# Kernel tuning notes

Hardware: AMD Instinct MI355X
Metric: run time of the kernel (lower is better)

## Reference

```python
import jax, jax.numpy as jnp
import numpy as np

IN = 128      # input_size
HID = 64      # fast_net hidden width
NFW = IN * HID + HID  # 8256 flat fast weights (layer1 then layer2)
B = 256


def setup_inputs() -> dict:
    key = jax.random.key(0)
    k1, k2, k3, k4 = jax.random.split(key, 4)
    x = jax.random.normal(k1, (B, 1, IN), dtype=jnp.float32)
    # updater network weights: Linear(IN, 2*NFW, bias=False) then Linear(2*NFW, NFW, bias=False)
    W1 = jax.random.normal(k2, (2 * NFW, IN), dtype=jnp.float32) * 0.02
    W2 = jax.random.normal(k3, (NFW, 2 * NFW), dtype=jnp.float32) * 0.02
    # initial flat fast weights, in (0,1) since the update squashes there
    fw0 = jax.random.uniform(k4, (NFW,), dtype=jnp.float32)
    return {"x": x, "W1": W1, "W2": W2, "fw0": fw0}


def reference(x, W1, W2, fw0):
    xs = x[:, 0, :]  # [B, IN]
    # updater network has no weight updates itself -> batch the two matmuls
    U = (xs @ W1.T) @ W2.T  # [B, NFW] per-sample weight updates
    gain, shift = jnp.float32(10.0), jnp.float32(0.5)

    def step(fw, inp):
        x_i, u_i = inp
        # update_func: 1 / (1 + exp(-10*(w + u - 0.5)))
        fw = jax.nn.sigmoid(gain * (fw + u_i - shift))
        w1 = fw[: IN * HID].reshape(HID, IN)   # fast layer 1 [HID, IN]
        w2 = fw[IN * HID:].reshape(1, HID)     # fast layer 2 [1, HID]
        pred = w2 @ jax.nn.relu(w1 @ x_i)      # [1]
        return fw, pred

    _, preds = jax.lax.scan(step, fw0, (xs, U))  # sequential over batch, state persists
    return preds  # [B, 1]
```

## Files before the change

kernel.cpp:

```cpp
#include <hip/hip_runtime.h>
#include <hip/hip_bf16.h>

#define IN_DIM 128
#define HID    64
#define NFW    8256
#define BATCH  256
#define K2     16512
#define BM     96
#define NMB    86
#define KSPLIT 6
#define NT_PER 43
#define GRID_M 516

typedef float f32x4 __attribute__((ext_vector_type(4)));
typedef short bf16x8 __attribute__((ext_vector_type(8)));

__device__ __forceinline__ unsigned int f2bf(float f) {
    union { float f; unsigned int u; } v; v.f = f;
    return (v.u + 0x7FFFu + ((v.u >> 16) & 1u)) >> 16;
}

__global__ __launch_bounds__(256) void k_prep_w1t(const float* __restrict__ W1,
                                                  unsigned short* __restrict__ W1T) {
    __shared__ float tile[64][IN_DIM + 1];
    const int kt = blockIdx.x;
    const int t  = threadIdx.x;
    const float* src = W1 + (size_t)kt * 64 * IN_DIM;
#pragma unroll
    for (int p = 0; p < 8; ++p) {
        int c4 = p * 256 + t;
        int e = c4 * 4;
        int row = e >> 7, col = e & 127;
        f32x4 v = *reinterpret_cast<const f32x4*>(src + row * IN_DIM + col);
        tile[row][col+0] = v.x; tile[row][col+1] = v.y;
        tile[row][col+2] = v.z; tile[row][col+3] = v.w;
    }
    __syncthreads();
    unsigned short* dst = W1T + (size_t)kt * (IN_DIM * 64);
#pragma unroll
    for (int it = 0; it < 4; ++it) {
        int c = it * 256 + t;
        int n = c >> 3, kl0 = (c & 7) * 8;
        uint4 w;
        w.x = f2bf(tile[kl0+0][n]) | (f2bf(tile[kl0+1][n]) << 16);
        w.y = f2bf(tile[kl0+2][n]) | (f2bf(tile[kl0+3][n]) << 16);
        w.z = f2bf(tile[kl0+4][n]) | (f2bf(tile[kl0+5][n]) << 16);
        w.w = f2bf(tile[kl0+6][n]) | (f2bf(tile[kl0+7][n]) << 16);
        *reinterpret_cast<uint4*>(dst + c * 8) = w;
    }
}

__global__ __launch_bounds__(256, 2) void k_gemm_M(const float* __restrict__ W2,
                                                   const unsigned short* __restrict__ W1T,
                                                   float* __restrict__ Mpart) {
    __shared__ __align__(16) unsigned char smem[57344];
    float* trs = reinterpret_cast<float*>(smem);

    const int t = threadIdx.x;
    const int lane = t & 63, wid = t >> 6;
    const int wm = wid >> 1, wn = wid & 1;
    const int l15 = lane & 15, l4 = (lane >> 4) & 3;

    const int b = blockIdx.x;
    const int xcd = b & 7, slot = b >> 3;
    const int p = (xcd < 4) ? (xcd * 65 + slot) : (260 + (xcd - 4) * 64 + slot);
    const int ks = p / NMB, mb = p % NMB;

    const int m0 = mb * BM;
    const int g0 = ks * NT_PER;
    const int kt0 = (p * 7) % NT_PER;

    const int ar  = t >> 3;
    const int ac  = (t & 7) * 8;
    const int asw = (ar & 7) << 4;
    const float* abase = W2 + (size_t)(m0 + ar) * K2 + (size_t)g0 * 64 + ac;
    const int bn  = t >> 1;
    const int bsw = (bn & 7) << 4;
    const unsigned short* bbase = W1T + (size_t)g0 * 8192 + bn * 64 + (t & 1) * 32;

    f32x4 sa0, sa1, sa2, sa3, sa4, sa5;
    uint4 sb0, sb1, sb2, sb3;
    f32x4 acc[3][4];
#pragma unroll
    for (int mf = 0; mf < 3; ++mf)
#pragma unroll
        for (int nf = 0; nf < 4; ++nf)
            acc[mf][nf] = (f32x4){0.f, 0.f, 0.f, 0.f};

#define LOADREGS(KT) {                                                         \
    const float* _ap = abase + (size_t)(KT) * 64;                              \
    sa0 = *reinterpret_cast<const f32x4*>(_ap);                                \
    sa1 = *reinterpret_cast<const f32x4*>(_ap + 4);                            \
    sa2 = *reinterpret_cast<const f32x4*>(_ap + (size_t)32 * K2);              \
    sa3 = *reinterpret_cast<const f32x4*>(_ap + (size_t)32 * K2 + 4);          \
    sa4 = *reinterpret_cast<const f32x4*>(_ap + (size_t)64 * K2);              \
    sa5 = *reinterpret_cast<const f32x4*>(_ap + (size_t)64 * K2 + 4);          \
    const unsigned short* _bp = bbase + (size_t)(KT) * 8192;                   \
    sb0 = *reinterpret_cast<const uint4*>(_bp);                                \
    sb1 = *reinterpret_cast<const uint4*>(_bp + 8);                            \
    sb2 = *reinterpret_cast<const uint4*>(_bp + 16);                           \
    sb3 = *reinterpret_cast<const uint4*>(_bp + 24); }

#define CVT16(W, LO, HI) { W.x = f2bf(LO.x) | (f2bf(LO.y) << 16);              \
                           W.y = f2bf(LO.z) | (f2bf(LO.w) << 16);              \
                           W.z = f2bf(HI.x) | (f2bf(HI.y) << 16);              \
                           W.w = f2bf(HI.z) | (f2bf(HI.w) << 16); }

#define STOREREGS(BUF) {                                                       \
    unsigned char* _Ash = smem + (BUF) * 12288;                                \
    unsigned char* _Bsh = smem + 24576 + (BUF) * 16384;                        \
    uint4 _w;                                                                  \
    const int _abyte = (t & 7) * 16;                                           \
    CVT16(_w, sa0, sa1);                                                       \
    *reinterpret_cast<uint4*>(&_Ash[(ar)      * 128 + (_abyte ^ asw)]) = _w;   \
    CVT16(_w, sa2, sa3);                                                       \
    *reinterpret_cast<uint4*>(&_Ash[(ar + 32) * 128 + (_abyte ^ asw)]) = _w;   \
    CVT16(_w, sa4, sa5);                                                       \
    *reinterpret_cast<uint4*>(&_Ash[(ar + 64) * 128 + (_abyte ^ asw)]) = _w;   \
    const int _bb = (t & 1) * 64;                                              \
    *reinterpret_cast<uint4*>(&_Bsh[bn * 128 + ((_bb)      ^ bsw)]) = sb0;     \
    *reinterpret_cast<uint4*>(&_Bsh[bn * 128 + ((_bb + 16) ^ bsw)]) = sb1;     \
    *reinterpret_cast<uint4*>(&_Bsh[bn * 128 + ((_bb + 32) ^ bsw)]) = sb2;     \
    *reinterpret_cast<uint4*>(&_Bsh[bn * 128 + ((_bb + 48) ^ bsw)]) = sb3; }

#define MFMA_PHASE(BUF) {                                                      \
    const unsigned char* _Ash = smem + (BUF) * 12288;                          \
    const unsigned char* _Bsh = smem + 24576 + (BUF) * 16384;                  \
    const int _fsw = (l15 & 7) << 4;                                           \
    _Pragma("unroll")                                                          \
    for (int kk = 0; kk < 2; ++kk) {                                           \
        const int _fc = (kk * 64 + l4 * 16) ^ _fsw;                            \
        bf16x8 af0 = *reinterpret_cast<const bf16x8*>(                         \
            &_Ash[(wm * 48 +  0 + l15) * 128 + _fc]);                          \
        bf16x8 af1 = *reinterpret_cast<const bf16x8*>(                         \
            &_Ash[(wm * 48 + 16 + l15) * 128 + _fc]);                          \
        bf16x8 af2 = *reinterpret_cast<const bf16x8*>(                         \
            &_Ash[(wm * 48 + 32 + l15) * 128 + _fc]);                          \
        bf16x8 bf0 = *reinterpret_cast<const bf16x8*>(                         \
            &_Bsh[(wn * 64 +  0 + l15) * 128 + _fc]);                          \
        bf16x8 bf1 = *reinterpret_cast<const bf16x8*>(                         \
            &_Bsh[(wn * 64 + 16 + l15) * 128 + _fc]);                          \
        bf16x8 bf2 = *reinterpret_cast<const bf16x8*>(                         \
            &_Bsh[(wn * 64 + 32 + l15) * 128 + _fc]);                          \
        bf16x8 bf3 = *reinterpret_cast<const bf16x8*>(                         \
            &_Bsh[(wn * 64 + 48 + l15) * 128 + _fc]);                          \
        acc[0][0] = __builtin_amdgcn_mfma_f32_16x16x32_bf16(af0, bf0, acc[0][0], 0, 0, 0); \
        acc[0][1] = __builtin_amdgcn_mfma_f32_16x16x32_bf16(af0, bf1, acc[0][1], 0, 0, 0); \
        acc[0][2] = __builtin_amdgcn_mfma_f32_16x16x32_bf16(af0, bf2, acc[0][2], 0, 0, 0); \
        acc[0][3] = __builtin_amdgcn_mfma_f32_16x16x32_bf16(af0, bf3, acc[0][3], 0, 0, 0); \
        acc[1][0] = __builtin_amdgcn_mfma_f32_16x16x32_bf16(af1, bf0, acc[1][0], 0, 0, 0); \
        acc[1][1] = __builtin_amdgcn_mfma_f32_16x16x32_bf16(af1, bf1, acc[1][1], 0, 0, 0); \
        acc[1][2] = __builtin_amdgcn_mfma_f32_16x16x32_bf16(af1, bf2, acc[1][2], 0, 0, 0); \
        acc[1][3] = __builtin_amdgcn_mfma_f32_16x16x32_bf16(af1, bf3, acc[1][3], 0, 0, 0); \
        acc[2][0] = __builtin_amdgcn_mfma_f32_16x16x32_bf16(af2, bf0, acc[2][0], 0, 0, 0); \
        acc[2][1] = __builtin_amdgcn_mfma_f32_16x16x32_bf16(af2, bf1, acc[2][1], 0, 0, 0); \
        acc[2][2] = __builtin_amdgcn_mfma_f32_16x16x32_bf16(af2, bf2, acc[2][2], 0, 0, 0); \
        acc[2][3] = __builtin_amdgcn_mfma_f32_16x16x32_bf16(af2, bf3, acc[2][3], 0, 0, 0); \
    } }

#define LBAR() { asm volatile("s_waitcnt lgkmcnt(0)" ::: "memory");            \
                 __builtin_amdgcn_s_barrier();                                 \
                 __builtin_amdgcn_sched_barrier(0); }

    int kreg = kt0;
    LOADREGS(kreg);
    STOREREGS(0);
    { int kn = kreg + 1; if (kn >= NT_PER) kn = 0; kreg = kn; }
    LOADREGS(kreg);
    LBAR();

    int cur = 0;
#pragma unroll 1
    for (int i = 0; i < NT_PER; ++i) {
        if (i + 1 < NT_PER) {
            STOREREGS(cur ^ 1);
        }
        if (i + 2 < NT_PER) {
            int kn = kreg + 1; if (kn >= NT_PER) kn = 0; kreg = kn;
            LOADREGS(kreg);
        }
        MFMA_PHASE(cur);
        LBAR();
        cur ^= 1;
    }

    float* outp = Mpart + (size_t)ks * ((size_t)NFW * IN_DIM) + (size_t)m0 * IN_DIM;
#pragma unroll 1
    for (int w = 0; w < 2; ++w) {
        __syncthreads();
        if (wm == w) {
#pragma unroll
            for (int mf = 0; mf < 3; ++mf)
#pragma unroll
                for (int nf = 0; nf < 4; ++nf)
#pragma unroll
                    for (int r = 0; r < 4; ++r)
                        trs[(mf * 16 + l4 * 4 + r) * 132 + wn * 64 + nf * 16 + l15] = acc[mf][nf][r];
        }
        __syncthreads();
#pragma unroll
        for (int q = 0; q < 6; ++q) {
            int idx = q * 256 + t;
            int rr = idx >> 5, c4 = (idx & 31) << 2;
            f32x4 v = *reinterpret_cast<const f32x4*>(&trs[rr * 132 + c4]);
            *reinterpret_cast<f32x4*>(outp + (size_t)(w * 48 + rr) * IN_DIM + c4) = v;
        }
    }
#undef LOADREGS
#undef CVT16
#undef STOREREGS
#undef MFMA_PHASE
#undef LBAR
}

__global__ __launch_bounds__(256) void k_reduce_M(const float* __restrict__ Mpart,
                                                  unsigned short* __restrict__ Mb) {
    const int idx = blockIdx.x * 256 + threadIdx.x;
    f32x4 s = (f32x4){0.f, 0.f, 0.f, 0.f};
#pragma unroll
    for (int ks = 0; ks < KSPLIT; ++ks) {
        f32x4 v = *reinterpret_cast<const f32x4*>(
            Mpart + (size_t)ks * ((size_t)NFW * IN_DIM) + (size_t)idx * 4);
        s.x += v.x; s.y += v.y; s.z += v.z; s.w += v.w;
    }
    uint2 o;
    o.x = f2bf(s.x) | (f2bf(s.y) << 16);
    o.y = f2bf(s.z) | (f2bf(s.w) << 16);
    *reinterpret_cast<uint2*>(Mb + (size_t)idx * 4) = o;
}

__global__ __launch_bounds__(256) void k_uchains(const float* __restrict__ xs,
                                                 const unsigned short* __restrict__ Mb,
                                                 const float* __restrict__ fw0,
                                                 float* __restrict__ FW) {
    __shared__ float Ulds[256][68];
    const int t = threadIdx.x, lane = t & 63, wid = t >> 6;
    const int l15 = lane & 15, l4 = (lane >> 4) & 3;
    const int j0 = blockIdx.x * 64;

    bf16x8 bfr[4][4];
#pragma unroll
    for (int kk = 0; kk < 4; ++kk)
#pragma unroll
        for (int nf = 0; nf < 4; ++nf)
            bfr[kk][nf] = *reinterpret_cast<const bf16x8*>(
                Mb + (size_t)(j0 + nf * 16 + l15) * IN_DIM + kk * 32 + l4 * 8);

#pragma unroll 1
    for (int ib = 0; ib < 4; ++ib) {
        const int i0 = wid * 64 + ib * 16;
        f32x4 acc[4];
#pragma unroll
        for (int nf = 0; nf < 4; ++nf) acc[nf] = (f32x4){0.f, 0.f, 0.f, 0.f};
#pragma unroll
        for (int kk = 0; kk < 4; ++kk) {
            const float* xp = xs + (size_t)(i0 + l15) * IN_DIM + kk * 32 + l4 * 8;
            f32x4 x0 = *reinterpret_cast<const f32x4*>(xp);
            f32x4 x1 = *reinterpret_cast<const f32x4*>(xp + 4);
            union { bf16x8 v; unsigned short s[8]; } af;
            af.s[0] = f2bf(x0.x); af.s[1] = f2bf(x0.y);
            af.s[2] = f2bf(x0.z); af.s[3] = f2bf(x0.w);
            af.s[4] = f2bf(x1.x); af.s[5] = f2bf(x1.y);
            af.s[6] = f2bf(x1.z); af.s[7] = f2bf(x1.w);
#pragma unroll
            for (int nf = 0; nf < 4; ++nf)
                acc[nf] = __builtin_amdgcn_mfma_f32_16x16x32_bf16(af.v, bfr[kk][nf], acc[nf], 0, 0, 0);
        }
#pragma unroll
        for (int nf = 0; nf < 4; ++nf)
#pragma unroll
            for (int r = 0; r < 4; ++r)
                Ulds[i0 + l4 * 4 + r][nf * 16 + l15] = acc[nf][r];
    }
    __syncthreads();

    if (wid == 0) {
        const int j = j0 + lane;
        float fw = fw0[j];
        float* fp = FW + j;
#pragma unroll 8
        for (int i = 0; i < BATCH; ++i) {
            float u = Ulds[i][lane];
            float z = 10.0f * (fw + u - 0.5f);
            fw = 1.0f / (1.0f + __expf(-z));
            fp[(size_t)i * NFW] = fw;
        }
    }
}

__global__ __launch_bounds__(256) void k_preds(const float* __restrict__ FW,
                                               const float* __restrict__ xs,
                                               float* __restrict__ out) {
    __shared__ float xsh[IN_DIM];
    __shared__ float hsh[HID];
    const int i = blockIdx.x, t = threadIdx.x;
    if (t < 32) {
        f32x4 v = *reinterpret_cast<const f32x4*>(xs + (size_t)i * IN_DIM + t * 4);
        xsh[t*4+0] = v.x; xsh[t*4+1] = v.y; xsh[t*4+2] = v.z; xsh[t*4+3] = v.w;
    }
    __syncthreads();
    const int k = t >> 2, q = t & 3;
    const float* fr = FW + (size_t)i * NFW + k * IN_DIM + q * 32;
    float p = 0.f;
#pragma unroll
    for (int m = 0; m < 8; ++m) {
        f32x4 v = *reinterpret_cast<const f32x4*>(fr + m * 4);
        const int d = q * 32 + m * 4;
        p += v.x * xsh[d] + v.y * xsh[d+1] + v.z * xsh[d+2] + v.w * xsh[d+3];
    }
    p += __shfl_xor(p, 1);
    p += __shfl_xor(p, 2);
    if (q == 0) hsh[k] = fmaxf(p, 0.f);
    __syncthreads();
    if (t < 64) {
        float v = FW[(size_t)i * NFW + IN_DIM * HID + t] * hsh[t];
        v += __shfl_xor(v, 1);  v += __shfl_xor(v, 2);  v += __shfl_xor(v, 4);
        v += __shfl_xor(v, 8);  v += __shfl_xor(v, 16); v += __shfl_xor(v, 32);
        if (t == 0) out[i] = v;
    }
}

extern "C" void kernel_launch(void* const* d_in, const int* in_sizes, int n_in,
                              void* d_out, int out_size, void* d_ws, size_t ws_size,
                              hipStream_t stream) {
    const float* x   = (const float*)d_in[0];
    const float* W1  = (const float*)d_in[1];
    const float* W2  = (const float*)d_in[2];
    const float* fw0 = (const float*)d_in[3];
    float* out = (float*)d_out;

    char* ws = (char*)d_ws;
    unsigned short* W1T   = (unsigned short*)(ws);
    float*          Mpart = (float*)(ws + 4227072);
    unsigned short* Mb    = (unsigned short*)(ws + 29589504);
    float*          FW    = (float*)(ws + 31703040);

    hipLaunchKernelGGL(k_prep_w1t, dim3(258),    dim3(256), 0, stream, W1, W1T);
    hipLaunchKernelGGL(k_gemm_M,   dim3(GRID_M), dim3(256), 0, stream, W2, W1T, Mpart);
    hipLaunchKernelGGL(k_reduce_M, dim3(1032),   dim3(256), 0, stream, Mpart, Mb);
    hipLaunchKernelGGL(k_uchains,  dim3(129),    dim3(256), 0, stream, x, Mb, fw0, FW);
    hipLaunchKernelGGL(k_preds,    dim3(256),    dim3(256), 0, stream, FW, x, out);
}
```

Baseline: 184.9 us.

## Read B fragments directly from global, double K-tile per stage, raise occupancy

The W2×W1T GEMM kernel stops staging the bf16 W1T operand through shared memory. Each wave now loads its B fragments straight from global/L2 inside the MFMA loop. The A tile now covers 128 K-columns per stage, so there are half as many barrier-separated iterations, split unevenly as 22 or 21 per K-split. Shared memory drops from 56KB to 48KB and launch bounds ask for 3 blocks per CU. In exchange, B is re-read per wave from cache, global load latency sits in the MFMA phase, and 12 A registers are held per thread, which may cause register pressure.

```diff
diff --git a/kernel.cpp b/kernel.cpp
--- a/kernel.cpp
+++ b/kernel.cpp
@@ -9,7 +9,6 @@
 #define BM     96
 #define NMB    86
 #define KSPLIT 6
-#define NT_PER 43
 #define GRID_M 516
 
 typedef float f32x4 __attribute__((ext_vector_type(4)));
@@ -50,10 +49,10 @@
     }
 }
 
-__global__ __launch_bounds__(256, 2) void k_gemm_M(const float* __restrict__ W2,
+__global__ __launch_bounds__(256, 3) void k_gemm_M(const float* __restrict__ W2,
                                                    const unsigned short* __restrict__ W1T,
                                                    float* __restrict__ Mpart) {
-    __shared__ __align__(16) unsigned char smem[57344];
+    __shared__ __align__(16) unsigned char smem[49152];
     float* trs = reinterpret_cast<float*>(smem);
 
     const int t = threadIdx.x;
@@ -67,19 +66,16 @@
     const int ks = p / NMB, mb = p % NMB;
 
     const int m0 = mb * BM;
-    const int g0 = ks * NT_PER;
-    const int kt0 = (p * 7) % NT_PER;
+    const int NT  = (ks < 3) ? 22 : 21;
+    const int g0p = ks * 21 + ((ks < 3) ? ks : 3);
+    const int kt0 = (p * 5) % NT;
 
     const int ar  = t >> 3;
-    const int ac  = (t & 7) * 8;
     const int asw = (ar & 7) << 4;
-    const float* abase = W2 + (size_t)(m0 + ar) * K2 + (size_t)g0 * 64 + ac;
-    const int bn  = t >> 1;
-    const int bsw = (bn & 7) << 4;
-    const unsigned short* bbase = W1T + (size_t)g0 * 8192 + bn * 64 + (t & 1) * 32;
-
-    f32x4 sa0, sa1, sa2, sa3, sa4, sa5;
-    uint4 sb0, sb1, sb2, sb3;
+    const float* abase = W2 + (size_t)(m0 + ar) * K2 + (t & 7) * 16;
+    const int boff = (wn * 64 + l15) * 64 + l4 * 8;
+
+    f32x4 sa0, sa1, sa2, sa3, sa4, sa5, sa6, sa7, sa8, sa9, sa10, sa11;
     f32x4 acc[3][4];
 #pragma unroll
     for (int mf = 0; mf < 3; ++mf)
@@ -87,63 +83,58 @@
         for (int nf = 0; nf < 4; ++nf)
             acc[mf][nf] = (f32x4){0.f, 0.f, 0.f, 0.f};
 
-#define LOADREGS(KT) {                                                         \
-    const float* _ap = abase + (size_t)(KT) * 64;                              \
-    sa0 = *reinterpret_cast<const f32x4*>(_ap);                                \
-    sa1 = *reinterpret_cast<const f32x4*>(_ap + 4);                            \
-    sa2 = *reinterpret_cast<const f32x4*>(_ap + (size_t)32 * K2);              \
-    sa3 = *reinterpret_cast<const f32x4*>(_ap + (size_t)32 * K2 + 4);          \
-    sa4 = *reinterpret_cast<const f32x4*>(_ap + (size_t)64 * K2);              \
-    sa5 = *reinterpret_cast<const f32x4*>(_ap + (size_t)64 * K2 + 4);          \
-    const unsigned short* _bp = bbase + (size_t)(KT) * 8192;                   \
-    sb0 = *reinterpret_cast<const uint4*>(_bp);                                \
-    sb1 = *reinterpret_cast<const uint4*>(_bp + 8);                            \
-    sb2 = *reinterpret_cast<const uint4*>(_bp + 16);                           \
-    sb3 = *reinterpret_cast<const uint4*>(_bp + 24); }
-
-#define CVT16(W, LO, HI) { W.x = f2bf(LO.x) | (f2bf(LO.y) << 16);              \
-                           W.y = f2bf(LO.z) | (f2bf(LO.w) << 16);              \
-                           W.z = f2bf(HI.x) | (f2bf(HI.y) << 16);              \
-                           W.w = f2bf(HI.z) | (f2bf(HI.w) << 16); }
-
-#define STOREREGS(BUF) {                                                       \
-    unsigned char* _Ash = smem + (BUF) * 12288;                                \
-    unsigned char* _Bsh = smem + 24576 + (BUF) * 16384;                        \
-    uint4 _w;                                                                  \
-    const int _abyte = (t & 7) * 16;                                           \
-    CVT16(_w, sa0, sa1);                                                       \
-    *reinterpret_cast<uint4*>(&_Ash[(ar)      * 128 + (_abyte ^ asw)]) = _w;   \
-    CVT16(_w, sa2, sa3);                                                       \
-    *reinterpret_cast<uint4*>(&_Ash[(ar + 32) * 128 + (_abyte ^ asw)]) = _w;   \
-    CVT16(_w, sa4, sa5);                                                       \
-    *reinterpret_cast<uint4*>(&_Ash[(ar + 64) * 128 + (_abyte ^ asw)]) = _w;   \
-    const int _bb = (t & 1) * 64;                                              \
-    *reinterpret_cast<uint4*>(&_Bsh[bn * 128 + ((_bb)      ^ bsw)]) = sb0;     \
-    *reinterpret_cast<uint4*>(&_Bsh[bn * 128 + ((_bb + 16) ^ bsw)]) = sb1;     \
-    *reinterpret_cast<uint4*>(&_Bsh[bn * 128 + ((_bb + 32) ^ bsw)]) = sb2;     \
-    *reinterpret_cast<uint4*>(&_Bsh[bn * 128 + ((_bb + 48) ^ bsw)]) = sb3; }
-
-#define MFMA_PHASE(BUF) {                                                      \
-    const unsigned char* _Ash = smem + (BUF) * 12288;                          \
-    const unsigned char* _Bsh = smem + 24576 + (BUF) * 16384;                  \
-    const int _fsw = (l15 & 7) << 4;                                           \
+#define LOADA(GP) {                                                            \
+    const float* _a0 = abase + (size_t)(GP) * 128;                             \
+    sa0  = *reinterpret_cast<const f32x4*>(_a0);                               \
+    sa1  = *reinterpret_cast<const f32x4*>(_a0 + 4);                           \
+    sa2  = *reinterpret_cast<const f32x4*>(_a0 + 8);                           \
+    sa3  = *reinterpret_cast<const f32x4*>(_a0 + 12);                          \
+    const float* _a1 = _a0 + (size_t)32 * K2;                                  \
+    sa4  = *reinterpret_cast<const f32x4*>(_a1);                               \
+    sa5  = *reinterpret_cast<const f32x4*>(_a1 + 4);                           \
+    sa6  = *reinterpret_cast<const f32x4*>(_a1 + 8);                           \
+    sa7  = *reinterpret_cast<const f32x4*>(_a1 + 12);                          \
+    const float* _a2 = _a0 + (size_t)64 * K2;                                  \
+    sa8  = *reinterpret_cast<const f32x4*>(_a2);                               \
+    sa9  = *reinterpret_cast<const f32x4*>(_a2 + 4);                           \
+    sa10 = *reinterpret_cast<const f32x4*>(_a2 + 8);                           \
+    sa11 = *reinterpret_cast<const f32x4*>(_a2 + 12); }
+
+#define PK(A,B) (f2bf(A) | (f2bf(B) << 16))
+#define STPASS(BASE, ROW, LO0, LO1, HI0, HI1) {                                \
+    uint4 _w0, _w1;                                                            \
+    _w0.x = PK(LO0.x, LO0.y); _w0.y = PK(LO0.z, LO0.w);                        \
+    _w0.z = PK(LO1.x, LO1.y); _w0.w = PK(LO1.z, LO1.w);                        \
+    _w1.x = PK(HI0.x, HI0.y); _w1.y = PK(HI0.z, HI0.w);                        \
+    _w1.z = PK(HI1.x, HI1.y); _w1.w = PK(HI1.z, HI1.w);                        \
+    const int _c = (t & 7) * 32;                                               \
+    *reinterpret_cast<uint4*>(&(BASE)[(ROW) * 256 + ((_c)      ^ asw)]) = _w0; \
+    *reinterpret_cast<uint4*>(&(BASE)[(ROW) * 256 + ((_c + 16) ^ asw)]) = _w1; }
+
+#define STOREA(BUF) {                                                          \
+    unsigned char* _Ash = smem + (BUF) * 24576;                                \
+    STPASS(_Ash, ar,      sa0, sa1, sa2,  sa3);                                \
+    STPASS(_Ash, ar + 32, sa4, sa5, sa6,  sa7);                                \
+    STPASS(_Ash, ar + 64, sa8, sa9, sa10, sa11); }
+
+#define MFMA_PAIR(BUF, GP) {                                                   \
+    const unsigned char* _Ash = smem + (BUF) * 24576;                          \
     _Pragma("unroll")                                                          \
-    for (int kk = 0; kk < 2; ++kk) {                                           \
-        const int _fc = (kk * 64 + l4 * 16) ^ _fsw;                            \
+    for (int kk = 0; kk < 4; ++kk) {                                           \
+        const unsigned short* _bp = W1T + (size_t)(2 * (GP) + (kk >> 1)) * 8192\
+                                    + boff + (kk & 1) * 32;                    \
+        bf16x8 bf0 = *reinterpret_cast<const bf16x8*>(_bp);                    \
+        bf16x8 bf1 = *reinterpret_cast<const bf16x8*>(_bp + 1024);             \
+        bf16x8 bf2 = *reinterpret_cast<const bf16x8*>(_bp + 2048);             \
+        bf16x8 bf3 = *reinterpret_cast<const bf16x8*>(_bp + 3072);             \
+        const int _fc = kk * 64 + l4 * 16;                                     \
+        const int _r0 = wm * 48 + l15;                                         \
         bf16x8 af0 = *reinterpret_cast<const bf16x8*>(                         \
-            &_Ash[(wm * 48 +  0 + l15) * 128 + _fc]);                          \
+            &_Ash[(_r0)      * 256 + (_fc ^ (((_r0)      & 7) << 4))]);        \
         bf16x8 af1 = *reinterpret_cast<const bf16x8*>(                         \
-            &_Ash[(wm * 48 + 16 + l15) * 128 + _fc]);                          \
+            &_Ash[(_r0 + 16) * 256 + (_fc ^ (((_r0 + 16) & 7) << 4))]);        \
         bf16x8 af2 = *reinterpret_cast<const bf16x8*>(                         \
-            &_Ash[(wm * 48 + 32 + l15) * 128 + _fc]);                          \
-        bf16x8 bf0 = *reinterpret_cast<const bf16x8*>(                         \
-            &_Bsh[(wn * 64 +  0 + l15) * 128 + _fc]);                          \
-        bf16x8 bf1 = *reinterpret_cast<const bf16x8*>(                         \
-            &_Bsh[(wn * 64 + 16 + l15) * 128 + _fc]);                          \
-        bf16x8 bf2 = *reinterpret_cast<const bf16x8*>(                         \
-            &_Bsh[(wn * 64 + 32 + l15) * 128 + _fc]);                          \
-        bf16x8 bf3 = *reinterpret_cast<const bf16x8*>(                         \
-            &_Bsh[(wn * 64 + 48 + l15) * 128 + _fc]);                          \
+            &_Ash[(_r0 + 32) * 256 + (_fc ^ (((_r0 + 32) & 7) << 4))]);        \
         acc[0][0] = __builtin_amdgcn_mfma_f32_16x16x32_bf16(af0, bf0, acc[0][0], 0, 0, 0); \
         acc[0][1] = __builtin_amdgcn_mfma_f32_16x16x32_bf16(af0, bf1, acc[0][1], 0, 0, 0); \
         acc[0][2] = __builtin_amdgcn_mfma_f32_16x16x32_bf16(af0, bf2, acc[0][2], 0, 0, 0); \
@@ -162,24 +153,25 @@
                  __builtin_amdgcn_s_barrier();                                 \
                  __builtin_amdgcn_sched_barrier(0); }
 
-    int kreg = kt0;
-    LOADREGS(kreg);
-    STOREREGS(0);
-    { int kn = kreg + 1; if (kn >= NT_PER) kn = 0; kreg = kn; }
-    LOADREGS(kreg);
+    int kc = kt0;
+    int klw = kt0 + 2 >= NT ? kt0 + 2 - NT : kt0 + 2;
+    LOADA(g0p + kc);
+    STOREA(0);
+    { int kn = kt0 + 1; if (kn >= NT) kn -= NT; LOADA(g0p + kn); }
     LBAR();
 
     int cur = 0;
 #pragma unroll 1
-    for (int i = 0; i < NT_PER; ++i) {
-        if (i + 1 < NT_PER) {
-            STOREREGS(cur ^ 1);
-        }
-        if (i + 2 < NT_PER) {
-            int kn = kreg + 1; if (kn >= NT_PER) kn = 0; kreg = kn;
-            LOADREGS(kreg);
-        }
-        MFMA_PHASE(cur);
+    for (int i = 0; i < NT; ++i) {
+        if (i + 1 < NT) {
+            STOREA(cur ^ 1);
+        }
+        if (i + 2 < NT) {
+            LOADA(g0p + klw);
+            klw = klw + 1 >= NT ? 0 : klw + 1;
+        }
+        MFMA_PAIR(cur, g0p + kc);
+        kc = kc + 1 >= NT ? 0 : kc + 1;
         LBAR();
         cur ^= 1;
     }
@@ -206,10 +198,11 @@
             *reinterpret_cast<f32x4*>(outp + (size_t)(w * 48 + rr) * IN_DIM + c4) = v;
         }
     }
-#undef LOADREGS
-#undef CVT16
-#undef STOREREGS
-#undef MFMA_PHASE
+#undef LOADA
+#undef PK
+#undef STPASS
+#undef STOREA
+#undef MFMA_PAIR
 #undef LBAR
 }
 
```

Measured after the change: 258.9 us. +40.0%, slower.
